# Kernel optimization log

Hardware: AMD Instinct MI355X
Metric: run time of the kernel (lower is better)

## Reference

```python
import jax, jax.numpy as jnp
import numpy as np

NUM_HEADS = 16


def _layernorm(x, g, b, eps=1e-5):
    mu = x.mean(-1, keepdims=True)
    var = ((x - mu) ** 2).mean(-1, keepdims=True)
    return (x - mu) / jnp.sqrt(var + eps) * g + b


def _mha(q_in, kv, w_qkv, b_qkv, w_o, b_o, key_pad, num_heads):
    # Faithful nn.MultiheadAttention (batch_first, eval mode, same key/value).
    B, Lq, D = q_in.shape
    Lk = kv.shape[1]
    dh = D // num_heads
    wq, wk, wv = jnp.split(w_qkv, 3, axis=0)
    bq, bk, bv = jnp.split(b_qkv, 3, axis=0)
    q = (q_in @ wq.T + bq).reshape(B, Lq, num_heads, dh).transpose(0, 2, 1, 3)
    k = (kv @ wk.T + bk).reshape(B, Lk, num_heads, dh).transpose(0, 2, 1, 3)
    v = (kv @ wv.T + bv).reshape(B, Lk, num_heads, dh).transpose(0, 2, 1, 3)
    scores = jnp.einsum('bhqd,bhkd->bhqk', q, k) / jnp.sqrt(jnp.asarray(dh, q.dtype))
    scores = jnp.where(key_pad[:, None, None, :], -jnp.inf, scores)
    attn = jax.nn.softmax(scores, axis=-1)
    out = jnp.einsum('bhqk,bhkd->bhqd', attn, v).transpose(0, 2, 1, 3).reshape(B, Lq, D)
    return out @ w_o.T + b_o


def _forward(queries, text_feat, region_feat, text_mask, region_mask,
             w_qkv_t, b_qkv_t, w_o_t, b_o_t,
             w_qkv_r, b_qkv_r, w_o_r, b_o_r,
             ln_g, ln_b, w1, b1, w2, b2, alpha):
    kp_t = text_mask == 0
    kp_r = region_mask == 0
    q1 = _mha(queries, text_feat, w_qkv_t, b_qkv_t, w_o_t, b_o_t, kp_t, NUM_HEADS)
    q = _layernorm(queries + q1, ln_g, ln_b)
    q2 = _mha(q, region_feat, w_qkv_r, b_qkv_r, w_o_r, b_o_r, kp_r, NUM_HEADS)
    q = _layernorm(q + q2, ln_g, ln_b)
    # manual masked cross-attentions (note: scaled by sqrt(hidden_dim), not head_dim)
    scale = jnp.sqrt(jnp.asarray(q.shape[-1], q.dtype))
    at = jnp.einsum('bqd,btd->bqt', q, text_feat) / scale
    at = jnp.where(kp_t[:, None, :], -jnp.inf, at)
    agg_t = jax.nn.softmax(at, axis=-1) @ text_feat
    ar = jnp.einsum('bqd,brd->bqr', q, region_feat) / scale
    ar = jnp.where(kp_r[:, None, :], -jnp.inf, ar)
    agg_r = jax.nn.softmax(ar, axis=-1) @ region_feat
    q = q + alpha * agg_r + (1.0 - alpha) * agg_t
    # FFN: Linear(D,4D) -> GELU (exact) -> Linear(4D,D), dropout inactive (eval)
    h = jax.nn.gelu(q @ w1.T + b1, approximate=False)
    return q + (h @ w2.T + b2)


def setup_inputs() -> dict:
    B, NQ, LT, LR, D = 16, 128, 512, 196, 1024
    ks = jax.random.split(jax.random.key(0), 24)
    s = 0.02
    lens_t = jax.random.randint(ks[10], (B,), LT // 2, LT + 1)
    lens_r = jax.random.randint(ks[11], (B,), LR // 2, LR + 1)
    return {
        'queries': jax.random.normal(ks[0], (B, NQ, D), jnp.float32),
        'text_feat': jax.random.normal(ks[1], (B, LT, D), jnp.float32),
        'region_feat': jax.random.normal(ks[2], (B, LR, D), jnp.float32),
        'text_mask': (jnp.arange(LT)[None, :] < lens_t[:, None]).astype(jnp.int32),
        'region_mask': (jnp.arange(LR)[None, :] < lens_r[:, None]).astype(jnp.int32),
        'w_qkv_t': s * jax.random.normal(ks[3], (3 * D, D), jnp.float32),
        'b_qkv_t': jnp.zeros((3 * D,), jnp.float32),
        'w_o_t': s * jax.random.normal(ks[4], (D, D), jnp.float32),
        'b_o_t': jnp.zeros((D,), jnp.float32),
        'w_qkv_r': s * jax.random.normal(ks[5], (3 * D, D), jnp.float32),
        'b_qkv_r': jnp.zeros((3 * D,), jnp.float32),
        'w_o_r': s * jax.random.normal(ks[6], (D, D), jnp.float32),
        'b_o_r': jnp.zeros((D,), jnp.float32),
        'ln_g': jnp.ones((D,), jnp.float32),
        'ln_b': jnp.zeros((D,), jnp.float32),
        'w1': s * jax.random.normal(ks[7], (4 * D, D), jnp.float32),
        'b1': jnp.zeros((4 * D,), jnp.float32),
        'w2': s * jax.random.normal(ks[8], (D, 4 * D), jnp.float32),
        'b2': jnp.zeros((D,), jnp.float32),
        'alpha': jnp.asarray(0.5, jnp.float32),
    }


def reference(queries, text_feat, region_feat, text_mask, region_mask,
              w_qkv_t, b_qkv_t, w_o_t, b_o_t,
              w_qkv_r, b_qkv_r, w_o_r, b_o_r,
              ln_g, ln_b, w1, b1, w2, b2, alpha):
    return _forward(queries, text_feat, region_feat, text_mask, region_mask,
                    w_qkv_t, b_qkv_t, w_o_t, b_o_t,
                    w_qkv_r, b_qkv_r, w_o_r, b_o_r,
                    ln_g, ln_b, w1, b1, w2, b2, alpha)
```

## Files before the change

### kernel.cpp

```cpp
#include <hip/hip_runtime.h>
#include <hip/hip_bf16.h>


typedef __attribute__((ext_vector_type(8))) short short8;
typedef __attribute__((ext_vector_type(4))) float f32x4;

#define DEV static __device__ __forceinline__

DEV unsigned short f2bf(float f) {
    unsigned u = __float_as_uint(f);
    u += 0x7fffu + ((u >> 16) & 1u);
    return (unsigned short)(u >> 16);
}
DEV float bf2f(unsigned short u) {
    return __uint_as_float(((unsigned)u) << 16);
}

struct CvtPack {
    const float* src[9];
    unsigned short* dst[9];
    long start16[10];
};

__global__ __launch_bounds__(256)
void k_cvt_multi(CvtPack p, long total16) {
    long i = (long)blockIdx.x * blockDim.x + threadIdx.x;
    long stride = (long)gridDim.x * blockDim.x;
    for (; i < total16; i += stride) {
        int t = 0;
#pragma unroll
        for (int k = 1; k < 9; ++k) t += (i >= p.start16[k]) ? 1 : 0;
        long off = i - p.start16[t];
        const f32x4* s = (const f32x4*)p.src[t] + off * 4;
        f32x4 a = s[0];
        f32x4 b = s[1];
        f32x4 c = s[2];
        f32x4 d = s[3];
        short8 o0, o1;
        o0[0] = (short)f2bf(a[0]); o0[1] = (short)f2bf(a[1]);
        o0[2] = (short)f2bf(a[2]); o0[3] = (short)f2bf(a[3]);
        o0[4] = (short)f2bf(b[0]); o0[5] = (short)f2bf(b[1]);
        o0[6] = (short)f2bf(b[2]); o0[7] = (short)f2bf(b[3]);
        o1[0] = (short)f2bf(c[0]); o1[1] = (short)f2bf(c[1]);
        o1[2] = (short)f2bf(c[2]); o1[3] = (short)f2bf(c[3]);
        o1[4] = (short)f2bf(d[0]); o1[5] = (short)f2bf(d[1]);
        o1[6] = (short)f2bf(d[2]); o1[7] = (short)f2bf(d[3]);
        short8* dp = (short8*)p.dst[t] + off * 2;
        dp[0] = o0;
        dp[1] = o1;
    }
}

__global__ __launch_bounds__(1024)
void k_gemm_nt256(const unsigned short* __restrict__ A, const unsigned short* __restrict__ B,
                  const float* __restrict__ bias,
                  float* __restrict__ outF, unsigned short* __restrict__ outB,
                  int M, int N, int K, int lda, int ldb, int ldc,
                  long sPart,
                  unsigned short* __restrict__ vT, int vColOff, long sVz, int vLd)
{
    __shared__ unsigned short smem[2 * 32768];

    unsigned gx = gridDim.x, gy = gridDim.y;
    unsigned nwg = gx * gy * gridDim.z;
    unsigned lin = (blockIdx.z * gy + blockIdx.y) * gx + blockIdx.x;
    unsigned bx = blockIdx.x, by = blockIdx.y, bz = blockIdx.z;
    if ((nwg & 7u) == 0u) {
        unsigned cpx = nwg >> 3;
        unsigned s = (lin & 7u) * cpx + (lin >> 3);
        bx = s % gx; unsigned r2 = s / gx;
        by = r2 % gy; bz = r2 / gy;
    }
    int s_k = (int)bz;
    const unsigned short* Ap = A + (long)s_k * K;
    const unsigned short* Bp = B + (long)s_k * K;
    float* outFp = outF ? outF + (long)s_k * sPart : nullptr;
    unsigned short* outBp = outB ? outB + (long)s_k * sPart : nullptr;

    int t = threadIdx.x;
    int wid = t >> 6, lane = t & 63;
    int lrow = lane & 15, kgrp = lane >> 4;
    int tm = by * 256, tn = bx * 256;
    int wm = (wid >> 2) * 64, wn = (wid & 3) * 64;

    auto stage = [&](int buf, int k0) {
#pragma unroll
        for (int r = 0; r < 2; ++r) {
            int d = r * 16384 + t * 16;
            int row = d >> 7;
            int colb = (d & 127) ^ ((row & 7) << 4);
            int gr = tm + row; if (gr > M - 1) gr = M - 1;
            const unsigned short* srcA = Ap + (long)gr * lda + k0 + (colb >> 1);
            unsigned short* dstA = smem + ((buf * 65536 + d) >> 1);
            __builtin_amdgcn_global_load_lds(
                (const __attribute__((address_space(1))) unsigned int*)srcA,
                (__attribute__((address_space(3))) unsigned int*)dstA, 16, 0, 0);
            int gn = tn + row; if (gn > N - 1) gn = N - 1;
            const unsigned short* srcB = Bp + (long)gn * ldb + k0 + (colb >> 1);
            unsigned short* dstB = smem + ((buf * 65536 + 32768 + d) >> 1);
            __builtin_amdgcn_global_load_lds(
                (const __attribute__((address_space(1))) unsigned int*)srcB,
                (__attribute__((address_space(3))) unsigned int*)dstB, 16, 0, 0);
        }
    };

    f32x4 acc[4][4] = {};
    int nt = K >> 6;

    stage(0, 0);

    for (int ti = 0; ti < nt; ++ti) {
        int cur = ti & 1;
        if (ti + 1 < nt) {
            stage(cur ^ 1, (ti + 1) << 6);
            asm volatile("s_waitcnt vmcnt(4)" ::: "memory");
        } else {
            asm volatile("s_waitcnt vmcnt(0)" ::: "memory");
        }
        __builtin_amdgcn_sched_barrier(0);
        __builtin_amdgcn_s_barrier();
        __builtin_amdgcn_sched_barrier(0);

        const char* Ab = (const char*)smem + cur * 65536;
        const char* Bb = Ab + 32768;
#pragma unroll
        for (int ks = 0; ks < 2; ++ks) {
            short8 a[4], bb[4];
            int kb = ks * 64 + kgrp * 16;
#pragma unroll
            for (int i = 0; i < 4; ++i) {
                int row = wm + i * 16 + lrow;
                a[i] = *(const short8*)(Ab + row * 128 + (kb ^ ((row & 7) << 4)));
            }
#pragma unroll
            for (int j = 0; j < 4; ++j) {
                int row = wn + j * 16 + lrow;
                bb[j] = *(const short8*)(Bb + row * 128 + (kb ^ ((row & 7) << 4)));
            }
#pragma unroll
            for (int i = 0; i < 4; ++i)
#pragma unroll
                for (int j = 0; j < 4; ++j)
                    acc[i][j] = __builtin_amdgcn_mfma_f32_16x16x32_bf16(a[i], bb[j], acc[i][j], 0, 0, 0);
        }
        __builtin_amdgcn_s_barrier();
    }

#pragma unroll
    for (int i = 0; i < 4; ++i) {
        int rbase = tm + wm + i * 16 + kgrp * 4;
#pragma unroll
        for (int j = 0; j < 4; ++j) {
            int c = tn + wn + j * 16 + lrow;
            if (c >= N) continue;
            float bv = bias ? bias[c] : 0.0f;
            float v[4];
#pragma unroll
            for (int e = 0; e < 4; ++e) v[e] = acc[i][j][e] + bv;
            if (vT && c >= vColOff) {
                if (rbase + 3 < M) {
                    int hh = (c - vColOff) >> 6, dd = (c - vColOff) & 63;
                    int bb2 = rbase >> 9, l = rbase & 511;
                    ushort4 o = { f2bf(v[0]), f2bf(v[1]), f2bf(v[2]), f2bf(v[3]) };
                    *(ushort4*)(vT + (long)(bb2 * 16 + hh) * sVz + (long)dd * vLd + l) = o;
                }
            } else {
#pragma unroll
                for (int e = 0; e < 4; ++e) {
                    int r = rbase + e;
                    if (r >= M) continue;
                    long oidx = (long)r * ldc + c;
                    if (outFp) outFp[oidx] = v[e];
                    if (outBp) outBp[oidx] = f2bf(v[e]);
                }
            }
        }
    }
}

__global__ __launch_bounds__(256)
void k_gemm_n64(const unsigned short* __restrict__ A, const unsigned short* __restrict__ B,
                const float* __restrict__ bias, const float* __restrict__ res,
                float* __restrict__ outF, unsigned short* __restrict__ outB,
                int K, int lda, int ldb, int ldc,
                int H, long sAb, long sAh, long sBz, long sCb, long sCh, int gelu,
                int S, long sPart)
{
    __shared__ unsigned short smem[5 * 6144];

    unsigned gx = gridDim.x, gy = gridDim.y;
    unsigned nwg = gx * gy * gridDim.z;
    unsigned lin = (blockIdx.z * gy + blockIdx.y) * gx + blockIdx.x;
    unsigned bx = blockIdx.x, by = blockIdx.y, bz = blockIdx.z;
    if ((nwg & 7u) == 0u) {
        unsigned cpx = nwg >> 3;
        unsigned s = (lin & 7u) * cpx + (lin >> 3);
        bx = s % gx; unsigned r2 = s / gx;
        by = r2 % gy; bz = r2 / gy;
    }

    int zz = (int)bz;
    int s_k = 0;
    if (S > 1) { s_k = zz % S; zz /= S; }
    int b = zz / H, h = zz - b * H;
    const unsigned short* Ap = A + (long)b * sAb + (long)h * sAh + (long)s_k * K;
    const unsigned short* Bp = B + (long)zz * sBz + (long)s_k * K;
    float* outFp = outF;
    unsigned short* outBp = outB;
    if (outBp && S > 1) outBp += (long)s_k * sPart;
    long offC = (long)b * sCb + (long)h * sCh;

    int t = threadIdx.x;
    int wid = t >> 6, lane = t & 63;
    int lrow = lane & 15, kgrp = lane >> 4;
    int tm = by * 128, tn = bx * 64;
    int wm = wid * 32;

    auto stage = [&](int buf, int k0) {
#pragma unroll
        for (int r = 0; r < 2; ++r) {
            int d = r * 4096 + t * 16;
            int row = d >> 6;
            int colb = (d & 63) ^ (((row >> 1) & 3) << 4);
            const unsigned short* srcA = Ap + (long)(tm + row) * lda + k0 + (colb >> 1);
            unsigned short* dstA = smem + ((buf * 12288 + d) >> 1);
            __builtin_amdgcn_global_load_lds(
                (const __attribute__((address_space(1))) unsigned int*)srcA,
                (__attribute__((address_space(3))) unsigned int*)dstA, 16, 0, 0);
        }
        {
            int d = t * 16;
            int row = d >> 6;
            int colb = (d & 63) ^ (((row >> 1) & 3) << 4);
            const unsigned short* srcB = Bp + (long)(tn + row) * ldb + k0 + (colb >> 1);
            unsigned short* dstB = smem + ((buf * 12288 + 8192 + d) >> 1);
            __builtin_amdgcn_global_load_lds(
                (const __attribute__((address_space(1))) unsigned int*)srcB,
                (__attribute__((address_space(3))) unsigned int*)dstB, 16, 0, 0);
        }
    };

    f32x4 acc[2][4] = {};
    int nt = K >> 5;

    for (int p = 0; p < 4 && p < nt; ++p) stage(p, p << 5);

    for (int ti = 0; ti < nt; ++ti) {
        int cur = ti % 5;
        int rem = nt - 1 - ti;
        if (rem >= 3)      asm volatile("s_waitcnt vmcnt(9)" ::: "memory");
        else if (rem == 2) asm volatile("s_waitcnt vmcnt(6)" ::: "memory");
        else if (rem == 1) asm volatile("s_waitcnt vmcnt(3)" ::: "memory");
        else               asm volatile("s_waitcnt vmcnt(0)" ::: "memory");
        __builtin_amdgcn_sched_barrier(0);
        __builtin_amdgcn_s_barrier();
        __builtin_amdgcn_sched_barrier(0);

        if (ti + 4 < nt) stage((ti + 4) % 5, (ti + 4) << 5);

        const char* Ab = (const char*)smem + cur * 12288;
        const char* Bb = Ab + 8192;
        short8 a[2], bb[4];
#pragma unroll
        for (int i = 0; i < 2; ++i) {
            int row = wm + i * 16 + lrow;
            a[i] = *(const short8*)(Ab + row * 64 + ((kgrp * 16) ^ (((row >> 1) & 3) << 4)));
        }
#pragma unroll
        for (int j = 0; j < 4; ++j) {
            int row = j * 16 + lrow;
            bb[j] = *(const short8*)(Bb + row * 64 + ((kgrp * 16) ^ (((row >> 1) & 3) << 4)));
        }
#pragma unroll
        for (int i = 0; i < 2; ++i)
#pragma unroll
            for (int j = 0; j < 4; ++j)
                acc[i][j] = __builtin_amdgcn_mfma_f32_16x16x32_bf16(a[i], bb[j], acc[i][j], 0, 0, 0);
    }

#pragma unroll
    for (int i = 0; i < 2; ++i) {
        int rbase = tm + wm + i * 16 + kgrp * 4;
#pragma unroll
        for (int j = 0; j < 4; ++j) {
            int c = tn + j * 16 + lrow;
            float bv = bias ? bias[c] : 0.0f;
#pragma unroll
            for (int e = 0; e < 4; ++e) {
                int r = rbase + e;
                long oidx = offC + (long)r * ldc + c;
                float v = acc[i][j][e] + bv;
                if (res) v += res[oidx];
                if (gelu) v = 0.5f * v * (1.0f + erff(v * 0.70710678118654752f));
                if (outFp) outFp[oidx] = v;
                if (outBp) outBp[oidx] = f2bf(v);
            }
        }
    }
}

template<bool GELU>
__global__ __launch_bounds__(256)
void k_gemm_nt(const unsigned short* __restrict__ A, const unsigned short* __restrict__ B,
               const float* __restrict__ bias, const float* __restrict__ res,
               float* __restrict__ outF, unsigned short* __restrict__ outB,
               int M, int N, int K, int lda, int ldb, int ldc,
               int H, long sAb, long sAh, long sBb, long sBh, long sCb, long sCh,
               float scale, int S, long sPart,
               unsigned short* __restrict__ vT, int vColOff, long sVz, int vLd, int rpb)
{
    __shared__ unsigned short smem[5 * 8192];

    unsigned gx = gridDim.x, gy = gridDim.y, gz = gridDim.z;
    unsigned nwg = gx * gy * gz;
    unsigned lin = (blockIdx.z * gy + blockIdx.y) * gx + blockIdx.x;
    unsigned bx = blockIdx.x, by = blockIdx.y, bz = blockIdx.z;
    if ((nwg & 7u) == 0u) {
        unsigned cpx = nwg >> 3;
        unsigned s = (lin & 7u) * cpx + (lin >> 3);
        bx = s % gx; unsigned r2 = s / gx;
        by = r2 % gy; bz = r2 / gy;
    }

    int zz = (int)bz;
    int s_k = 0;
    if (S > 1) { s_k = zz % S; zz /= S; }
    int b = zz / H, h = zz - b * H;
    const unsigned short* Ap = A + (long)b * sAb + (long)h * sAh + (long)s_k * K;
    const unsigned short* Bp = B + (long)b * sBb + (long)h * sBh + (long)s_k * K;
    float* outFp = outF;
    if (outFp && S > 1) outFp += (long)s_k * sPart;
    unsigned short* outBp = outB;
    if (outBp && S > 1) outBp += (long)s_k * sPart;
    long offC = (long)b * sCb + (long)h * sCh;

    int t    = threadIdx.x;
    int wid  = t >> 6;
    int lane = t & 63;
    int lrow = lane & 15;
    int kgrp = lane >> 4;

    int tm = by * 128;
    int tn = bx * 128;
    int wm = (wid >> 1) * 64;
    int wn = (wid & 1) * 64;

    auto stage = [&](int buf, int k0) {
#pragma unroll
        for (int r = 0; r < 2; ++r) {
            int d = r * 4096 + t * 16;
            int row = d >> 6;
            int colb = (d & 63) ^ (((row >> 1) & 3) << 4);
            int gr = tm + row; if (gr > M - 1) gr = M - 1;
            const unsigned short* srcA = Ap + (long)gr * lda + k0 + (colb >> 1);
            unsigned short* dstA = smem + ((buf * 16384 + r * 4096 + wid * 1024) >> 1);
            __builtin_amdgcn_global_load_lds(
                (const __attribute__((address_space(1))) unsigned int*)srcA,
                (__attribute__((address_space(3))) unsigned int*)dstA, 16, 0, 0);
            int gn = tn + row; if (gn > N - 1) gn = N - 1;
            const unsigned short* srcB = Bp + (long)gn * ldb + k0 + (colb >> 1);
            unsigned short* dstB = smem + ((buf * 16384 + 8192 + r * 4096 + wid * 1024) >> 1);
            __builtin_amdgcn_global_load_lds(
                (const __attribute__((address_space(1))) unsigned int*)srcB,
                (__attribute__((address_space(3))) unsigned int*)dstB, 16, 0, 0);
        }
    };

    f32x4 acc[4][4] = {};
    int nt = K >> 5;

    for (int p = 0; p < 4 && p < nt; ++p) stage(p, p << 5);

    for (int ti = 0; ti < nt; ++ti) {
        int cur = ti % 5;
        int rem = nt - 1 - ti;
        if (rem >= 3)      asm volatile("s_waitcnt vmcnt(12)" ::: "memory");
        else if (rem == 2) asm volatile("s_waitcnt vmcnt(8)"  ::: "memory");
        else if (rem == 1) asm volatile("s_waitcnt vmcnt(4)"  ::: "memory");
        else               asm volatile("s_waitcnt vmcnt(0)"  ::: "memory");
        __builtin_amdgcn_sched_barrier(0);
        __builtin_amdgcn_s_barrier();
        __builtin_amdgcn_sched_barrier(0);

        if (ti + 4 < nt) stage((ti + 4) % 5, (ti + 4) << 5);

        const char* Ab = (const char*)smem + cur * 16384;
        const char* Bb = Ab + 8192;
        short8 a[4], bb[4];
#pragma unroll
        for (int i = 0; i < 4; ++i) {
            int row = wm + i * 16 + lrow;
            a[i] = *(const short8*)(Ab + row * 64 + ((kgrp * 16) ^ (((row >> 1) & 3) << 4)));
        }
#pragma unroll
        for (int j = 0; j < 4; ++j) {
            int row = wn + j * 16 + lrow;
            bb[j] = *(const short8*)(Bb + row * 64 + ((kgrp * 16) ^ (((row >> 1) & 3) << 4)));
        }
#pragma unroll
        for (int i = 0; i < 4; ++i)
#pragma unroll
            for (int j = 0; j < 4; ++j)
                acc[i][j] = __builtin_amdgcn_mfma_f32_16x16x32_bf16(a[i], bb[j], acc[i][j], 0, 0, 0);
    }

#pragma unroll
    for (int i = 0; i < 4; ++i) {
        int rbase = tm + wm + i * 16 + kgrp * 4;
#pragma unroll
        for (int j = 0; j < 4; ++j) {
            int c = tn + wn + j * 16 + lrow;
            if (c >= N) continue;
            float bv = bias ? bias[c] : 0.0f;
            if (vT && c >= vColOff) {
                int hh = (c - vColOff) >> 6, dd = (c - vColOff) & 63;
#pragma unroll
                for (int e = 0; e < 4; ++e) {
                    int r = rbase + e;
                    if (r >= M) continue;
                    float v = acc[i][j][e] * scale + bv;
                    int bb2 = r / rpb, l = r - bb2 * rpb;
                    vT[(long)(bb2 * 16 + hh) * sVz + (long)dd * vLd + l] = f2bf(v);
                }
                continue;
            }
#pragma unroll
            for (int e = 0; e < 4; ++e) {
                int r = rbase + e;
                if (r >= M) continue;
                float v = acc[i][j][e] * scale + bv;
                long oidx = offC + (long)r * ldc + c;
                if (res) v += res[oidx];
                if (GELU) v = 0.5f * v * (1.0f + erff(v * 0.70710678118654752f));
                if (outFp) outFp[oidx] = v;
                if (outBp) outBp[oidx] = f2bf(v);
            }
        }
    }
}

__global__ __launch_bounds__(256)
void k_redux_b(const unsigned short* __restrict__ part, long sPart, int S,
               const float* __restrict__ bias, const float* __restrict__ res,
               float* __restrict__ outF, unsigned short* __restrict__ outB,
               long n8, int ldc8, int gelu)
{
    long i = (long)blockIdx.x * blockDim.x + threadIdx.x;
    long stride = (long)gridDim.x * blockDim.x;
    for (; i < n8; i += stride) {
        long e0 = i * 8;
        float v[8];
        short8 p0 = *(const short8*)(part + e0);
#pragma unroll
        for (int k = 0; k < 8; ++k) v[k] = bf2f((unsigned short)p0[k]);
        for (int s = 1; s < S; ++s) {
            short8 ps = *(const short8*)(part + e0 + (long)s * sPart);
#pragma unroll
            for (int k = 0; k < 8; ++k) v[k] += bf2f((unsigned short)ps[k]);
        }
        if (bias) {
            int c = (int)(i % ldc8) * 8;
            float4 b0 = *(const float4*)(bias + c);
            float4 b1 = *(const float4*)(bias + c + 4);
            v[0] += b0.x; v[1] += b0.y; v[2] += b0.z; v[3] += b0.w;
            v[4] += b1.x; v[5] += b1.y; v[6] += b1.z; v[7] += b1.w;
        }
        if (res) {
            float4 r0 = *(const float4*)(res + e0);
            float4 r1 = *(const float4*)(res + e0 + 4);
            v[0] += r0.x; v[1] += r0.y; v[2] += r0.z; v[3] += r0.w;
            v[4] += r1.x; v[5] += r1.y; v[6] += r1.z; v[7] += r1.w;
        }
        if (gelu) {
#pragma unroll
            for (int k = 0; k < 8; ++k)
                v[k] = 0.5f * v[k] * (1.0f + erff(v[k] * 0.70710678118654752f));
        }
        if (outF) {
            float4 o0 = { v[0], v[1], v[2], v[3] };
            float4 o1 = { v[4], v[5], v[6], v[7] };
            *(float4*)(outF + e0) = o0;
            *(float4*)(outF + e0 + 4) = o1;
        }
        if (outB) {
            short8 o;
#pragma unroll
            for (int k = 0; k < 8; ++k) o[k] = (short)f2bf(v[k]);
            *(short8*)(outB + e0) = o;
        }
    }
}

__global__ __launch_bounds__(256)
void k_redux_ln_b(const unsigned short* __restrict__ part, long sPart, int S,
                  const float* __restrict__ bias, const float* __restrict__ res,
                  const float* __restrict__ g, const float* __restrict__ bt,
                  float* __restrict__ yf, unsigned short* __restrict__ yb)
{
    int row = blockIdx.x;
    int t = threadIdx.x;
    int lane = t & 63, wid = t >> 6;
    long base = (long)row * 1024 + t * 4;

    ushort4 p0 = *(const ushort4*)(part + base);
    float v0 = bf2f(p0.x), v1 = bf2f(p0.y), v2 = bf2f(p0.z), v3 = bf2f(p0.w);
    for (int s = 1; s < S; ++s) {
        ushort4 ps = *(const ushort4*)(part + base + (long)s * sPart);
        v0 += bf2f(ps.x); v1 += bf2f(ps.y); v2 += bf2f(ps.z); v3 += bf2f(ps.w);
    }
    float4 bv = *(const float4*)(bias + t * 4);
    v0 += bv.x; v1 += bv.y; v2 += bv.z; v3 += bv.w;
    float4 rv = *(const float4*)(res + base);
    v0 += rv.x; v1 += rv.y; v2 += rv.z; v3 += rv.w;

    float s1 = v0 + v1 + v2 + v3;
    float s2 = v0 * v0 + v1 * v1 + v2 * v2 + v3 * v3;
#pragma unroll
    for (int d = 32; d > 0; d >>= 1) { s1 += __shfl_xor(s1, d, 64); s2 += __shfl_xor(s2, d, 64); }
    __shared__ float rs[4], rss[4];
    if (lane == 0) { rs[wid] = s1; rss[wid] = s2; }
    __syncthreads();
    s1 = rs[0] + rs[1] + rs[2] + rs[3];
    s2 = rss[0] + rss[1] + rss[2] + rss[3];
    float mu  = s1 * (1.0f / 1024.0f);
    float var = s2 * (1.0f / 1024.0f) - mu * mu;
    float inv = rsqrtf(var + 1e-5f);

    float4 gv = *(const float4*)(g + t * 4);
    float4 btv = *(const float4*)(bt + t * 4);
    float o0 = (v0 - mu) * inv * gv.x + btv.x;
    float o1 = (v1 - mu) * inv * gv.y + btv.y;
    float o2 = (v2 - mu) * inv * gv.z + btv.z;
    float o3 = (v3 - mu) * inv * gv.w + btv.w;
    float4 of = { o0, o1, o2, o3 };
    ushort4 ob = { f2bf(o0), f2bf(o1), f2bf(o2), f2bf(o3) };
    *(float4*)(yf + base) = of;
    *(ushort4*)(yb + base) = ob;
}

__global__ __launch_bounds__(256)
void k_tr(const unsigned short* __restrict__ in, unsigned short* __restrict__ out,
          int R, int ldin, int ldout,
          int H, long sIb, long sIh, long sOz)
{
    __shared__ unsigned short tile[32][33];
    int z = blockIdx.z;
    int b = z / H, h = z - b * H;
    const unsigned short* ip = in + (long)b * sIb + (long)h * sIh;
    unsigned short* op = out + (long)z * sOz;
    int t = threadIdx.x;
    int cl = t & 31, rl = t >> 5;
    int c0 = blockIdx.x * 32, r0 = blockIdx.y * 32;
#pragma unroll
    for (int i = 0; i < 4; ++i) {
        int r = r0 + rl + i * 8;
        unsigned short v = 0;
        if (r < R) v = ip[(long)r * ldin + (c0 + cl)];
        tile[rl + i * 8][cl] = v;
    }
    __syncthreads();
#pragma unroll
    for (int i = 0; i < 4; ++i) {
        int orow = c0 + rl + i * 8;
        int ocol = r0 + cl;
        op[(long)orow * ldout + ocol] = tile[cl][rl + i * 8];
    }
}

__global__ __launch_bounds__(256)
void k_softmax_w(const float* __restrict__ sc, long sPart, int S,
                 unsigned short* __restrict__ P,
                 const int* __restrict__ mask, int L, int Lpad,
                 int ld_sc, int ld_p, int rows_per_batch, int nrows)
{
    int gw = (int)((blockIdx.x * 256 + threadIdx.x) >> 6);
    if (gw >= nrows) return;
    int lane = threadIdx.x & 63;
    int b = gw / rows_per_batch;
    const float* p = sc + (long)gw * ld_sc;
    unsigned short* po = P + (long)gw * ld_p;
    const int* mrow = mask + (long)b * L;

    int nch = (Lpad + 255) >> 8;
    float v[2][4];
    float mx = -INFINITY;
#pragma unroll
    for (int c = 0; c < 2; ++c) {
        if (c >= nch) { v[c][0]=v[c][1]=v[c][2]=v[c][3] = -INFINITY; continue; }
        int j = c * 256 + lane * 4;
        if (j < L) {
            float4 x = *(const float4*)(p + j);
            for (int s = 1; s < S; ++s) {
                float4 y = *(const float4*)(p + j + (long)s * sPart);
                x.x += y.x; x.y += y.y; x.z += y.z; x.w += y.w;
            }
            int4 m = *(const int4*)(mrow + j);
            v[c][0] = m.x ? x.x : -INFINITY;
            v[c][1] = m.y ? x.y : -INFINITY;
            v[c][2] = m.z ? x.z : -INFINITY;
            v[c][3] = m.w ? x.w : -INFINITY;
        } else {
            v[c][0]=v[c][1]=v[c][2]=v[c][3] = -INFINITY;
        }
        mx = fmaxf(mx, fmaxf(fmaxf(v[c][0], v[c][1]), fmaxf(v[c][2], v[c][3])));
    }
#pragma unroll
    for (int d = 32; d > 0; d >>= 1) mx = fmaxf(mx, __shfl_xor(mx, d, 64));

    float sum = 0.f;
#pragma unroll
    for (int c = 0; c < 2; ++c)
#pragma unroll
        for (int k = 0; k < 4; ++k) {
            float e = (v[c][k] == -INFINITY) ? 0.0f : __expf(v[c][k] - mx);
            v[c][k] = e;
            sum += e;
        }
#pragma unroll
    for (int d = 32; d > 0; d >>= 1) sum += __shfl_xor(sum, d, 64);
    float inv = 1.0f / sum;

#pragma unroll
    for (int c = 0; c < 2; ++c) {
        if (c >= nch) continue;
        int j = c * 256 + lane * 4;
        if (j < Lpad) {
            ushort4 o;
            o.x = f2bf(v[c][0] * inv);
            o.y = f2bf(v[c][1] * inv);
            o.z = f2bf(v[c][2] * inv);
            o.w = f2bf(v[c][3] * inv);
            *(ushort4*)(po + j) = o;
        }
    }
}

__global__ void k_combine_b(float* __restrict__ qf, unsigned short* __restrict__ qb,
                            const unsigned short* __restrict__ aggtp,
                            const unsigned short* __restrict__ aggrp,
                            const float* __restrict__ alpha, long n4, long sPart, int S)
{
    float a = *alpha;
    long i = (long)blockIdx.x * blockDim.x + threadIdx.x;
    long stride = (long)gridDim.x * blockDim.x;
    for (; i < n4; i += stride) {
        long e0 = i * 4;
        float st[4] = {0.f, 0.f, 0.f, 0.f}, sr[4] = {0.f, 0.f, 0.f, 0.f};
        for (int s = 0; s < S; ++s) {
            ushort4 pt = *(const ushort4*)(aggtp + e0 + (long)s * sPart);
            ushort4 pr = *(const ushort4*)(aggrp + e0 + (long)s * sPart);
            st[0] += bf2f(pt.x); st[1] += bf2f(pt.y); st[2] += bf2f(pt.z); st[3] += bf2f(pt.w);
            sr[0] += bf2f(pr.x); sr[1] += bf2f(pr.y); sr[2] += bf2f(pr.z); sr[3] += bf2f(pr.w);
        }
        float4 q = *(const float4*)(qf + e0);
        float v0 = q.x + a * sr[0] + (1.0f - a) * st[0];
        float v1 = q.y + a * sr[1] + (1.0f - a) * st[1];
        float v2 = q.z + a * sr[2] + (1.0f - a) * st[2];
        float v3 = q.w + a * sr[3] + (1.0f - a) * st[3];
        float4 of = { v0, v1, v2, v3 };
        ushort4 ob = { f2bf(v0), f2bf(v1), f2bf(v2), f2bf(v3) };
        *(float4*)(qf + e0) = of;
        *(ushort4*)(qb + e0) = ob;
    }
}

extern "C" void kernel_launch(void* const* d_in, const int* in_sizes, int n_in,
                              void* d_out, int out_size, void* d_ws, size_t ws_size,
                              hipStream_t stream)
{
    const float* queries = (const float*)d_in[0];
    const float* text    = (const float*)d_in[1];
    const float* region  = (const float*)d_in[2];
    const int*   tmask   = (const int*)d_in[3];
    const int*   rmask   = (const int*)d_in[4];
    const float* w_qkv_t = (const float*)d_in[5];
    const float* b_qkv_t = (const float*)d_in[6];
    const float* w_o_t   = (const float*)d_in[7];
    const float* b_o_t   = (const float*)d_in[8];
    const float* w_qkv_r = (const float*)d_in[9];
    const float* b_qkv_r = (const float*)d_in[10];
    const float* w_o_r   = (const float*)d_in[11];
    const float* b_o_r   = (const float*)d_in[12];
    const float* ln_g    = (const float*)d_in[13];
    const float* ln_b    = (const float*)d_in[14];
    const float* w1      = (const float*)d_in[15];
    const float* b1      = (const float*)d_in[16];
    const float* w2      = (const float*)d_in[17];
    const float* b2      = (const float*)d_in[18];
    const float* alpha   = (const float*)d_in[19];

    const int Bn = 16, NQ = 128, LT = 512, LR = 196, D = 1024, H = 16;
    const int LRp = 256;
    const int MQ = Bn * NQ;
    const int MT = Bn * LT;
    const int MR = Bn * LR;

    char* ws = (char*)d_ws;
    size_t off = 0;
    auto alloc = [&](size_t bytes) -> void* {
        void* p = ws + off;
        off = (off + bytes + 255) & ~(size_t)255;
        return p;
    };
    unsigned short* qb     = (unsigned short*)alloc((size_t)MQ * D * 2);
    unsigned short* tb     = (unsigned short*)alloc((size_t)MT * D * 2);
    unsigned short* rb     = (unsigned short*)alloc((size_t)MR * D * 2);
    unsigned short* wqkvtb = (unsigned short*)alloc((size_t)3 * D * D * 2);
    unsigned short* wotb   = (unsigned short*)alloc((size_t)D * D * 2);
    unsigned short* wqkvrb = (unsigned short*)alloc((size_t)3 * D * D * 2);
    unsigned short* worb   = (unsigned short*)alloc((size_t)D * D * 2);
    unsigned short* w1b    = (unsigned short*)alloc((size_t)4 * D * D * 2);
    unsigned short* w2b    = (unsigned short*)alloc((size_t)4 * D * D * 2);
    unsigned short* ktv    = (unsigned short*)alloc((size_t)MT * 2 * D * 2);
    unsigned short* krv    = (unsigned short*)alloc((size_t)MR * 2 * D * 2);
    unsigned short* vtT    = (unsigned short*)alloc((size_t)Bn * H * 64 * LT * 2);
    unsigned short* vrT    = (unsigned short*)alloc((size_t)Bn * H * 64 * LRp * 2);
    unsigned short* qp     = (unsigned short*)alloc((size_t)MQ * D * 2);
    unsigned short* ao     = (unsigned short*)alloc((size_t)MQ * D * 2);
    unsigned short* qlnb   = (unsigned short*)alloc((size_t)MQ * D * 2);
    float* qlf  = (float*)alloc((size_t)MQ * D * 4);
    float* sc   = (float*)alloc((size_t)Bn * H * NQ * LT * 4);
    if (off > ws_size) return;

    unsigned short* tbT = ktv;
    unsigned short* rbT = ktv + (size_t)Bn * D * LT;
    float* sct = sc;
    float* scr = sc;
    unsigned short* Pt = (unsigned short*)sc;
    unsigned short* Pr = (unsigned short*)(sc + 1 * 1048576);
    float* atp   = sc + 2 * 1048576;
    float* arp   = sc + 6 * 1048576;
    unsigned short* aggtp_b = (unsigned short*)((char*)sc + (size_t)32 * 1048576);
    unsigned short* aggrp_b = (unsigned short*)((char*)sc + (size_t)48 * 1048576);
    unsigned short* hb = (unsigned short*)sc;
    unsigned short* part_qb  = (unsigned short*)sc;
    unsigned short* part_f1b = ktv;

    const long PQ = (long)MQ * D;

    {
        CvtPack pk;
        const float* srcs[9] = { queries, text, region, w_qkv_t, w_o_t, w_qkv_r, w_o_r, w1, w2 };
        unsigned short* dsts[9] = { qb, tb, rb, wqkvtb, wotb, wqkvrb, worb, w1b, w2b };
        long ns[9] = { (long)MQ * D, (long)MT * D, (long)MR * D, (long)3 * D * D,
                       (long)D * D, (long)3 * D * D, (long)D * D, (long)4 * D * D,
                       (long)4 * D * D };
        long acc16 = 0;
        pk.start16[0] = 0;
        for (int i = 0; i < 9; ++i) {
            pk.src[i] = srcs[i]; pk.dst[i] = dsts[i];
            acc16 += ns[i] / 16;
            pk.start16[i + 1] = acc16;
        }
        k_cvt_multi<<<2048, 256, 0, stream>>>(pk, acc16);
    }

    auto NT = [&](const unsigned short* A, const unsigned short* Bm, const float* bias,
                  const float* res, float* oF, unsigned short* oB,
                  int M, int N, int K, int lda, int ldb, int ldc,
                  int Hh, long sAb, long sAh, long sBb, long sBh, long sCb, long sCh,
                  int batch, float scale, bool gelu, int S = 1, long sPart = 0,
                  unsigned short* vT = nullptr, int vColOff = 0, long sVz = 0,
                  int vLd = 0, int rpb = 1) {
        dim3 g((N + 127) / 128, (M + 127) / 128, batch * S);
        if (gelu)
            k_gemm_nt<true><<<g, 256, 0, stream>>>(A, Bm, bias, res, oF, oB, M, N, K,
                lda, ldb, ldc, Hh, sAb, sAh, sBb, sBh, sCb, sCh, scale, S, sPart,
                vT, vColOff, sVz, vLd, rpb);
        else
            k_gemm_nt<false><<<g, 256, 0, stream>>>(A, Bm, bias, res, oF, oB, M, N, K,
                lda, ldb, ldc, Hh, sAb, sAh, sBb, sBh, sCb, sCh, scale, S, sPart,
                vT, vColOff, sVz, vLd, rpb);
    };
    auto NT256 = [&](const unsigned short* A, const unsigned short* Bm, const float* bias,
                     float* oF, unsigned short* oB, int M, int N, int Kc,
                     int lda, int ldb, int ldc, int S, long sPart,
                     unsigned short* vT = nullptr, int vColOff = 0, long sVz = 0,
                     int vLd = 0) {
        dim3 g((N + 255) / 256, (M + 255) / 256, S);
        k_gemm_nt256<<<g, 1024, 0, stream>>>(A, Bm, bias, oF, oB, M, N, Kc,
                                             lda, ldb, ldc, sPart, vT, vColOff, sVz, vLd);
    };
    auto N64 = [&](const unsigned short* A, const unsigned short* Bm, const float* bias,
                   const float* res, float* oF, unsigned short* oB,
                   int M, int N, int K, int lda, int ldb, int ldc,
                   int Hh, long sAb, long sAh, long sBz, long sCb, long sCh, int Z,
                   int gelu = 0, int S = 1, long sPart = 0) {
        dim3 g(N / 64, M / 128, Z * S);
        k_gemm_n64<<<g, 256, 0, stream>>>(A, Bm, bias, res, oF, oB, K,
                                          lda, ldb, ldc, Hh, sAb, sAh, sBz, sCb, sCh,
                                          gelu, S, sPart);
    };
    auto REDUXB = [&](const unsigned short* part, long sPart, int S, const float* bias,
                      const float* res, float* oF, unsigned short* oB,
                      long total, int ldc, int gelu) {
        long n8 = total / 8;
        int blocks = (int)((n8 + 255) / 256);
        if (blocks > 2048) blocks = 2048;
        k_redux_b<<<blocks, 256, 0, stream>>>(part, sPart, S, bias, res, oF, oB,
                                              n8, ldc / 8, gelu);
    };
    auto SMAX = [&](const float* scp, long sPart, int S, unsigned short* P,
                    const int* mask, int L, int Lpad, int ld_sc, int ld_p,
                    int rpb, int nrows) {
        int blocks = (nrows + 3) / 4;
        k_softmax_w<<<blocks, 256, 0, stream>>>(scp, sPart, S, P, mask, L, Lpad,
                                                ld_sc, ld_p, rpb, nrows);
    };

    NT256(tb, wqkvtb + (long)D * D, b_qkv_t + D, nullptr, ktv,
          MT, 2 * D, D, D, D, 2 * D, 1, 0,
          vtT, D, (long)64 * LT, LT);
    NT(rb, wqkvrb + (long)D * D, b_qkv_r + D, nullptr, nullptr, krv,
       MR, 2 * D, D, D, D, 2 * D, 1,0,0,0,0,0,0, 1, 1.0f, false, 1, 0,
       vrT, D, (long)64 * LRp, LRp, LR);

    N64(qb, wqkvtb, b_qkv_t, nullptr, nullptr, qp, MQ, D, D, D, D, D,
        1, 0, 0, 0, 0, 0, 1);
    NT(qp, ktv, nullptr, nullptr, sct, nullptr, NQ, LT, 64, D, 2 * D, LT,
       H, (long)NQ * D, 64, (long)LT * 2 * D, 64, (long)H * NQ * LT, (long)NQ * LT,
       Bn * H, 0.125f, false);
    SMAX(sct, 0, 1, (unsigned short*)sct, tmask, LT, LT, LT, 2 * LT,
         H * NQ, Bn * H * NQ);
    N64((const unsigned short*)sct, vtT, nullptr, nullptr, nullptr, ao,
        NQ, 64, LT, 2 * LT, LT, D,
        H, (long)H * NQ * 2 * LT, (long)NQ * 2 * LT, (long)64 * LT,
        (long)NQ * D, 64, Bn * H);
    N64(ao, wotb, nullptr, nullptr, nullptr, part_qb, MQ, D, D, D, D, D,
        1, 0, 0, 0, 0, 0, 1);
    k_redux_ln_b<<<MQ, 256, 0, stream>>>(part_qb, PQ, 1, b_o_t, queries,
                                         ln_g, ln_b, qlf, qlnb);

    N64(qlnb, wqkvrb, b_qkv_r, nullptr, nullptr, qp, MQ, D, D, D, D, D,
        1, 0, 0, 0, 0, 0, 1);
    NT(qp, krv, nullptr, nullptr, scr, nullptr, NQ, LR, 64, D, 2 * D, LRp,
       H, (long)NQ * D, 64, (long)LR * 2 * D, 64, (long)H * NQ * LRp, (long)NQ * LRp,
       Bn * H, 0.125f, false);
    SMAX(scr, 0, 1, (unsigned short*)scr, rmask, LR, LRp, LRp, 2 * LRp,
         H * NQ, Bn * H * NQ);
    N64((const unsigned short*)scr, vrT, nullptr, nullptr, nullptr, ao,
        NQ, 64, LRp, 2 * LRp, LRp, D,
        H, (long)H * NQ * 2 * LRp, (long)NQ * 2 * LRp, (long)64 * LRp,
        (long)NQ * D, 64, Bn * H);
    N64(ao, worb, nullptr, nullptr, nullptr, part_qb, MQ, D, D, D, D, D,
        1, 0, 0, 0, 0, 0, 1);
    k_redux_ln_b<<<MQ, 256, 0, stream>>>(part_qb, PQ, 1, b_o_r, qlf,
                                         ln_g, ln_b, qlf, qlnb);

    {
        dim3 g1(D / 32, LT / 32, Bn);
        k_tr<<<g1, 256, 0, stream>>>(tb, tbT, LT, D, LT, 1, (long)LT * D, 0, (long)D * LT);
        dim3 g2(D / 32, LRp / 32, Bn);
        k_tr<<<g2, 256, 0, stream>>>(rb, rbT, LR, D, LRp, 1, (long)LR * D, 0, (long)D * LRp);
    }
    NT(qlnb, tb, nullptr, nullptr, atp, nullptr, NQ, LT, 256, D, D, LT,
       1, (long)NQ * D, 0, (long)LT * D, 0, (long)NQ * LT, 0, Bn, 0.03125f, false,
       4, (long)Bn * NQ * LT);
    SMAX(atp, (long)Bn * NQ * LT, 4, Pt, tmask, LT, LT, LT, LT, NQ, Bn * NQ);
    NT(Pt, tbT, nullptr, nullptr, nullptr, aggtp_b, NQ, D, 256, LT, LT, D,
       1, (long)NQ * LT, 0, (long)D * LT, 0, (long)NQ * D, 0, Bn, 1.0f, false,
       2, PQ);
    NT(qlnb, rb, nullptr, nullptr, arp, nullptr, NQ, LR, 256, D, D, LRp,
       1, (long)NQ * D, 0, (long)LR * D, 0, (long)NQ * LRp, 0, Bn, 0.03125f, false,
       4, (long)Bn * NQ * LRp);
    SMAX(arp, (long)Bn * NQ * LRp, 4, Pr, rmask, LR, LRp, LRp, LRp, NQ, Bn * NQ);
    NT(Pr, rbT, nullptr, nullptr, nullptr, aggrp_b, NQ, D, 128, LRp, LRp, D,
       1, (long)NQ * LRp, 0, (long)D * LRp, 0, (long)NQ * D, 0, Bn, 1.0f, false,
       2, PQ);

    k_combine_b<<<2048, 256, 0, stream>>>(qlf, qlnb, aggtp_b, aggrp_b, alpha,
                                          (long)MQ * D / 4, PQ, 2);

    NT256(qlnb, w1b, nullptr, nullptr, part_f1b, MQ, 4 * D, 512,
          D, D, 4 * D, 2, (long)MQ * 4 * D);
    REDUXB(part_f1b, (long)MQ * 4 * D, 2, b1, nullptr, nullptr, hb,
           (long)MQ * 4 * D, 4 * D, 1);
    N64(hb, w2b, b2, qlf, (float*)d_out, nullptr, MQ, D, 4 * D, 4 * D, 4 * D, D,
        1, 0, 0, 0, 0, 0, 1);
}
```

Measured before the change: 471.4 us.

## Fuse per-head QK^T scores and masked softmax into one MFMA kernel

Adds a templated kernel that, per (batch, head), loads Q (128 rows) and all keys into LDS, computes QK^T with bf16 MFMA, and does the masked softmax in registers using cross-wave reductions through shared memory. It writes bf16 probabilities directly. This replaces the separate score GEMM plus softmax launches for both MHA blocks, removing the fp32 score round-trip through global memory and one launch each. It assumes NQ=128, head dim 64, and L at most NJ*64. Only Bn*H blocks of 1024 threads are launched, which may limit occupancy.

Result: faster. 428.2 us (-9.1%).

```diff
diff --git a/kernel.cpp b/kernel.cpp
--- a/kernel.cpp
+++ b/kernel.cpp
@@ -48,6 +48,137 @@
         short8* dp = (short8*)p.dst[t] + off * 2;
         dp[0] = o0;
         dp[1] = o1;
+    }
+}
+
+template<int NJ>
+__global__ __launch_bounds__(1024)
+void k_qks(const unsigned short* __restrict__ Q, const unsigned short* __restrict__ Km,
+           unsigned short* __restrict__ P, const int* __restrict__ mask,
+           int L, int lda, int ldb, int H, long sQb, long sKb, float scale)
+{
+    const int Lpad = NJ * 64;
+    __shared__ unsigned short sm[8192 + 32768];
+    __shared__ float redm[128][4];
+    __shared__ float reds[128][4];
+
+    int z = blockIdx.z;
+    int b = z / H, h = z - b * H;
+    const unsigned short* Qp = Q + (long)b * sQb + (long)h * 64;
+    const unsigned short* Kp = Km + (long)b * sKb + (long)h * 64;
+    unsigned short* Pp = P + (long)z * 128 * Lpad;
+    const int* mrow = mask + (long)b * L;
+
+    int t = threadIdx.x;
+    int wid = t >> 6, lane = t & 63;
+    int lrow = lane & 15, kgrp = lane >> 4;
+    int wm = (wid >> 2) * 32;
+    int wn = (wid & 3) * (NJ * 16);
+
+    {
+        int d = t * 16;
+        int row = d >> 7;
+        int colb = (d & 127) ^ ((row & 7) << 4);
+        __builtin_amdgcn_global_load_lds(
+            (const __attribute__((address_space(1))) unsigned int*)(Qp + (long)row * lda + (colb >> 1)),
+            (__attribute__((address_space(3))) unsigned int*)(sm + (d >> 1)), 16, 0, 0);
+    }
+#pragma unroll
+    for (int r = 0; r < NJ / 2; ++r) {
+        int full = r * 16384 + t * 16;
+        int row = full >> 7;
+        int colb = (full & 127) ^ ((row & 7) << 4);
+        int kr = row; if (kr > L - 1) kr = L - 1;
+        __builtin_amdgcn_global_load_lds(
+            (const __attribute__((address_space(1))) unsigned int*)(Kp + (long)kr * ldb + (colb >> 1)),
+            (__attribute__((address_space(3))) unsigned int*)(sm + 8192 + (full >> 1)), 16, 0, 0);
+    }
+    asm volatile("s_waitcnt vmcnt(0)" ::: "memory");
+    __builtin_amdgcn_sched_barrier(0);
+    __syncthreads();
+
+    const char* Qs = (const char*)sm;
+    const char* Ks = (const char*)(sm + 8192);
+    f32x4 acc[2][NJ] = {};
+#pragma unroll
+    for (int ks = 0; ks < 2; ++ks) {
+        int kb = ks * 64 + kgrp * 16;
+        short8 a[2], bb[NJ];
+#pragma unroll
+        for (int i = 0; i < 2; ++i) {
+            int row = wm + i * 16 + lrow;
+            a[i] = *(const short8*)(Qs + row * 128 + (kb ^ ((row & 7) << 4)));
+        }
+#pragma unroll
+        for (int j = 0; j < NJ; ++j) {
+            int row = wn + j * 16 + lrow;
+            bb[j] = *(const short8*)(Ks + row * 128 + (kb ^ ((row & 7) << 4)));
+        }
+#pragma unroll
+        for (int i = 0; i < 2; ++i)
+#pragma unroll
+            for (int j = 0; j < NJ; ++j)
+                acc[i][j] = __builtin_amdgcn_mfma_f32_16x16x32_bf16(a[i], bb[j], acc[i][j], 0, 0, 0);
+    }
+
+    bool okj[NJ];
+#pragma unroll
+    for (int j = 0; j < NJ; ++j) {
+        int c = wn + j * 16 + lrow;
+        okj[j] = (c < L) && (mrow[c] != 0);
+    }
+
+    int nw = wid & 3;
+#pragma unroll
+    for (int i = 0; i < 2; ++i) {
+#pragma unroll
+        for (int e = 0; e < 4; ++e) {
+            float m = -INFINITY;
+#pragma unroll
+            for (int j = 0; j < NJ; ++j)
+                if (okj[j]) m = fmaxf(m, acc[i][j][e] * scale);
+#pragma unroll
+            for (int d = 1; d < 16; d <<= 1) m = fmaxf(m, __shfl_xor(m, d, 64));
+            int rl = wm + i * 16 + kgrp * 4 + e;
+            if (lrow == 0) redm[rl][nw] = m;
+        }
+    }
+    __syncthreads();
+
+#pragma unroll
+    for (int i = 0; i < 2; ++i) {
+#pragma unroll
+        for (int e = 0; e < 4; ++e) {
+            int rl = wm + i * 16 + kgrp * 4 + e;
+            float m = fmaxf(fmaxf(redm[rl][0], redm[rl][1]),
+                            fmaxf(redm[rl][2], redm[rl][3]));
+            float s = 0.f;
+#pragma unroll
+            for (int j = 0; j < NJ; ++j) {
+                float ev = okj[j] ? __expf(acc[i][j][e] * scale - m) : 0.0f;
+                acc[i][j][e] = ev;
+                s += ev;
+            }
+#pragma unroll
+            for (int d = 1; d < 16; d <<= 1) s += __shfl_xor(s, d, 64);
+            if (lrow == 0) reds[rl][nw] = s;
+        }
+    }
+    __syncthreads();
+
+#pragma unroll
+    for (int i = 0; i < 2; ++i) {
+#pragma unroll
+        for (int e = 0; e < 4; ++e) {
+            int rl = wm + i * 16 + kgrp * 4 + e;
+            float inv = 1.0f / (reds[rl][0] + reds[rl][1] + reds[rl][2] + reds[rl][3]);
+            unsigned short* pr = Pp + (long)rl * Lpad;
+#pragma unroll
+            for (int j = 0; j < NJ; ++j) {
+                int c = wn + j * 16 + lrow;
+                pr[c] = f2bf(acc[i][j][e] * inv);
+            }
+        }
     }
 }
 
@@ -724,8 +855,7 @@
 
     unsigned short* tbT = ktv;
     unsigned short* rbT = ktv + (size_t)Bn * D * LT;
-    float* sct = sc;
-    float* scr = sc;
+    unsigned short* Patt = (unsigned short*)sc;
     unsigned short* Pt = (unsigned short*)sc;
     unsigned short* Pr = (unsigned short*)(sc + 1 * 1048576);
     float* atp   = sc + 2 * 1048576;
@@ -817,14 +947,12 @@
 
     N64(qb, wqkvtb, b_qkv_t, nullptr, nullptr, qp, MQ, D, D, D, D, D,
         1, 0, 0, 0, 0, 0, 1);
-    NT(qp, ktv, nullptr, nullptr, sct, nullptr, NQ, LT, 64, D, 2 * D, LT,
-       H, (long)NQ * D, 64, (long)LT * 2 * D, 64, (long)H * NQ * LT, (long)NQ * LT,
-       Bn * H, 0.125f, false);
-    SMAX(sct, 0, 1, (unsigned short*)sct, tmask, LT, LT, LT, 2 * LT,
-         H * NQ, Bn * H * NQ);
-    N64((const unsigned short*)sct, vtT, nullptr, nullptr, nullptr, ao,
-        NQ, 64, LT, 2 * LT, LT, D,
-        H, (long)H * NQ * 2 * LT, (long)NQ * 2 * LT, (long)64 * LT,
+    k_qks<8><<<dim3(1, 1, Bn * H), 1024, 0, stream>>>(
+        qp, ktv, Patt, tmask, LT, D, 2 * D, H,
+        (long)NQ * D, (long)LT * 2 * D, 0.125f);
+    N64(Patt, vtT, nullptr, nullptr, nullptr, ao,
+        NQ, 64, LT, LT, LT, D,
+        H, (long)H * NQ * LT, (long)NQ * LT, (long)64 * LT,
         (long)NQ * D, 64, Bn * H);
     N64(ao, wotb, nullptr, nullptr, nullptr, part_qb, MQ, D, D, D, D, D,
         1, 0, 0, 0, 0, 0, 1);
@@ -833,14 +961,12 @@
 
     N64(qlnb, wqkvrb, b_qkv_r, nullptr, nullptr, qp, MQ, D, D, D, D, D,
         1, 0, 0, 0, 0, 0, 1);
-    NT(qp, krv, nullptr, nullptr, scr, nullptr, NQ, LR, 64, D, 2 * D, LRp,
-       H, (long)NQ * D, 64, (long)LR * 2 * D, 64, (long)H * NQ * LRp, (long)NQ * LRp,
-       Bn * H, 0.125f, false);
-    SMAX(scr, 0, 1, (unsigned short*)scr, rmask, LR, LRp, LRp, 2 * LRp,
-         H * NQ, Bn * H * NQ);
-    N64((const unsigned short*)scr, vrT, nullptr, nullptr, nullptr, ao,
-        NQ, 64, LRp, 2 * LRp, LRp, D,
-        H, (long)H * NQ * 2 * LRp, (long)NQ * 2 * LRp, (long)64 * LRp,
+    k_qks<4><<<dim3(1, 1, Bn * H), 1024, 0, stream>>>(
+        qp, krv, Patt, rmask, LR, D, 2 * D, H,
+        (long)NQ * D, (long)LR * 2 * D, 0.125f);
+    N64(Patt, vrT, nullptr, nullptr, nullptr, ao,
+        NQ, 64, LRp, LRp, LRp, D,
+        H, (long)H * NQ * LRp, (long)NQ * LRp, (long)64 * LRp,
         (long)NQ * D, 64, Bn * H);
     N64(ao, worb, nullptr, nullptr, nullptr, part_qb, MQ, D, D, D, D, D,
         1, 0, 0, 0, 0, 0, 1);
```
